# Kernel tuning notes

Measured on AMD Instinct MI355X. Metric: run time of the kernel, lower is better.

Reference implementation:

```python
import jax, jax.numpy as jnp
import numpy as np

WSIZE = 8
HEADS = 6
CYC_SHIFT = True


def _relative_index(w):
    # same math as SelfAttention._getRelativeIndex
    coords = np.stack(np.meshgrid(np.arange(w), np.arange(w), indexing='ij'))
    coords = coords.reshape(2, -1)                      # [2, w*w]
    rel = coords[:, :, None] - coords[:, None, :]       # [2, N, N]
    rel = rel.copy()
    rel[0] += w - 1
    rel[0] *= 2 * w - 1
    rel[1] += w - 1
    return (rel[0] + rel[1]).reshape(-1)                # [N*N]


def _shift_mask(H, W, w):
    # same math as CycShftWndwPartition._mask
    part = np.zeros((H, W), dtype=np.float32)
    slices = [slice(0, -w), slice(-w, -w // 2), slice(-w // 2, None)]
    idx = 0
    for hs in slices:
        for ws_ in slices:
            part[hs, ws_] = idx
            idx += 1
    part = part.reshape(H // w, w, W // w, w).transpose(0, 2, 1, 3).reshape(-1, w * w)
    diff = part[:, None, :] - part[:, :, None]          # [nW, N, N]
    return np.where(diff != 0, -100.0, 0.0).astype(np.float32)


def setup_inputs() -> dict:
    key = jax.random.key(0)
    k0, k1, k2, k3, k4 = jax.random.split(key, 5)
    B, H, W, C = 4, 384, 384, 60
    return {
        'cvrt_img': jax.random.normal(k0, (B, H, W, C), dtype=jnp.float32),
        'qkv_w': jax.random.normal(k1, (C, 3 * C), dtype=jnp.float32) * 0.05,
        'bias_matrix': jax.random.normal(k2, ((2 * WSIZE - 1) ** 2, HEADS), dtype=jnp.float32) * 0.02,
        'proj_w': jax.random.normal(k3, (C, C), dtype=jnp.float32) * 0.05,
        'proj_b': jax.random.normal(k4, (C,), dtype=jnp.float32) * 0.02,
    }


def reference(cvrt_img, qkv_w, bias_matrix, proj_w, proj_b):
    B, H, W, C = cvrt_img.shape
    w = WSIZE
    N = w * w
    d = C // HEADS
    nWh, nWw = H // w, W // w
    WNum = nWh * nWw

    # cyclic shift + window partition
    if CYC_SHIFT:
        x = jnp.roll(cvrt_img, shift=(-(w // 2), -(w // 2)), axis=(1, 2))
        mask = jnp.asarray(_shift_mask(H, W, w))        # [WNum, N, N]
    else:
        x = cvrt_img
        mask = jnp.zeros((WNum, N, N), dtype=cvrt_img.dtype)
    windows = x.reshape(B, nWh, w, nWw, w, C).transpose(0, 1, 3, 2, 4, 5)
    windows = windows.reshape(B * WNum, N, C)

    # windowed multi-head self-attention
    qkv = (windows @ qkv_w).reshape(B * WNum, N, 3, HEADS, d)
    qkv = qkv.transpose(2, 0, 3, 1, 4)                  # [3, Bw, H, N, d]
    q, k, v = qkv[0], qkv[1], qkv[2]
    attn = jnp.einsum('bhnd,bhmd->bhnm', q, k) / (d ** 0.5)

    rel_idx = jnp.asarray(_relative_index(w))
    bias = bias_matrix[rel_idx].reshape(N, N, HEADS).transpose(2, 0, 1)  # [H, N, N]
    attn = attn + bias[None]

    attn = attn.reshape(B, WNum, HEADS, N, N) + mask[None, :, None]
    attn = jax.nn.softmax(attn.reshape(B * WNum, HEADS, N, N), axis=-1)

    out = jnp.einsum('bhnm,bhmd->bhnd', attn, v)        # [Bw, H, N, d]
    out = out.transpose(0, 2, 1, 3).reshape(B * WNum, N, C)
    new_windows = out @ proj_w + proj_b

    # un-partition + reverse cyclic shift
    y = new_windows.reshape(B, nWh, nWw, w, w, C).transpose(0, 1, 3, 2, 4, 5)
    y = y.reshape(B, H, W, C)
    if CYC_SHIFT:
        y = jnp.roll(y, shift=(w // 2, w // 2), axis=(1, 2))
    return y
```

## Files before the change

kernel.cpp:

```cpp
#include <hip/hip_runtime.h>
#include <hip/hip_bf16.h>

#define IMG    384
#define CDIM   60
#define NWIN   48
#define WNUM   (NWIN * NWIN)

typedef short  bf16x8 __attribute__((ext_vector_type(8)));
typedef float  f32x4  __attribute__((ext_vector_type(4)));
union Frag { int4 i4; bf16x8 b8; };

#define MFMA(a, b, c) __builtin_amdgcn_mfma_f32_16x16x32_bf16((a), (b), (c), 0, 0, 0)

#define WS_QKVF  0
#define WS_VF    24576
#define WS_PROJF 36864
#define WS_BIASF 45056

#define SCALE_L2E (0.31622776601683794f * 1.4426950408889634f)
#define MASK_L2E  144.26950408889634f
#define LOG2E     1.4426950408889634f

__device__ __forceinline__ unsigned short f2bf(float f) {
    unsigned int u = __float_as_uint(f);
    unsigned int r = u + 0x7fffu + ((u >> 16) & 1u);
    return (unsigned short)(r >> 16);
}
__device__ __forceinline__ unsigned int pk2bf(float a, float b) {
    union { __hip_bfloat162 h; unsigned int u; } c;
    c.h = __float22bfloat162_rn(float2{a, b});
    return c.u;
}
__device__ __forceinline__ int regionOf(int x) {
    return (x < IMG - 8) ? 0 : ((x < IMG - 4) ? 1 : 2);
}
__device__ __forceinline__ int swz(int row, int byteoff) {
    return (row * 128 + byteoff) ^ ((row & 7) << 4);
}
__device__ __forceinline__ int4 qk_frag(const unsigned short* buf, int tok, int h, int g) {
    if (g == 0) return *(const int4*)((const char*)buf + swz(tok, h * 16));
    if (g == 1) {
        int v = *(const int*)((const char*)buf + swz(tok, 96 + h * 4));
        return int4{v, 0, 0, 0};
    }
    return int4{0, 0, 0, 0};
}

__global__ void swin_prep(const float* __restrict__ qw,
                          const float* __restrict__ pw,
                          const float* __restrict__ bias,
                          unsigned char* __restrict__ ws)
{
    int t = blockIdx.x * 256 + threadIdx.x;
    if (t < 1536) {
        int lane = t & 63, f = t >> 6;
        int mt = f >> 1, ks = f & 1;
        int h = mt >> 1, type = mt & 1;
        int d = lane & 15, g8 = lane >> 4;
        unsigned short v8[8];
        #pragma unroll
        for (int jj = 0; jj < 8; ++jj) {
            int c = ks * 32 + g8 * 8 + jj;
            v8[jj] = f2bf((d < 10 && c < 60) ? qw[c * 180 + type * 60 + h * 10 + d] : 0.f);
        }
        int4 p;
        p.x = v8[0] | (v8[1] << 16);  p.y = v8[2] | (v8[3] << 16);
        p.z = v8[4] | (v8[5] << 16);  p.w = v8[6] | (v8[7] << 16);
        *(int4*)(ws + WS_QKVF + t * 16) = p;
    } else if (t < 2304) {
        int t2 = t - 1536;
        int lane = t2 & 63, f = t2 >> 6;
        int h = f >> 1, ks = f & 1;
        int d = lane & 15, g8 = lane >> 4;
        unsigned short v8[8];
        #pragma unroll
        for (int jj = 0; jj < 8; ++jj) {
            int c = ks * 32 + g8 * 8 + jj;
            v8[jj] = f2bf((d < 10 && c < 60) ? qw[c * 180 + 120 + h * 10 + d] : 0.f);
        }
        int4 p;
        p.x = v8[0] | (v8[1] << 16);  p.y = v8[2] | (v8[3] << 16);
        p.z = v8[4] | (v8[5] << 16);  p.w = v8[6] | (v8[7] << 16);
        *(int4*)(ws + WS_VF + t2 * 16) = p;
    } else if (t < 2816) {
        int t2 = t - 2304;
        int lane = t2 & 63, fq = t2 >> 6;
        int m = fq >> 1, ks = fq & 1;
        int c = m * 16 + (lane & 15);
        int g8 = lane >> 4;
        unsigned short v8[8];
        #pragma unroll
        for (int jj = 0; jj < 8; ++jj) {
            int cc = ks * 32 + g8 * 8 + jj;
            v8[jj] = f2bf((c < 60 && cc < 60) ? pw[cc * 60 + c] : 0.f);
        }
        int4 p;
        p.x = v8[0] | (v8[1] << 16);  p.y = v8[2] | (v8[3] << 16);
        p.z = v8[4] | (v8[5] << 16);  p.w = v8[6] | (v8[7] << 16);
        *(int4*)(ws + WS_PROJF + t2 * 16) = p;
    } else if (t < 2816 + 24576) {
        int idx = t - 2816;
        int h = idx >> 12, r = idx & 4095;
        int i = r >> 6, j = r & 63;
        int yi = i >> 3, xi = i & 7, yj = j >> 3, xj = j & 7;
        int ridx = (yi - yj + 7) * 15 + (xi - xj + 7);
        ((float*)(ws + WS_BIASF))[h * 4096 + i * 64 + j] = bias[ridx * 6 + h] * LOG2E;
    }
}

__global__ __launch_bounds__(256, 4)
void swin_mfma(const float* __restrict__ img,
               const float* __restrict__ pbias,
               const unsigned char* __restrict__ ws,
               float* __restrict__ out)
{
    __shared__ __align__(16) unsigned short uni [64 * 64];
    __shared__ __align__(16) unsigned short qall[64 * 64];
    __shared__ __align__(16) unsigned short kall[64 * 64];
    __shared__ __align__(16) unsigned short vall[61 * 64];
    __shared__ __align__(16) unsigned short osb [64 * 64];

    const int tid  = threadIdx.x;
    const int lane = tid & 63;
    const int wid  = __builtin_amdgcn_readfirstlane(tid >> 6);
    const int l15  = lane & 15;
    const int g    = lane >> 4;
    const int dl   = (32 + l15) << 2;

    const int bid = blockIdx.x;
    const int b   = bid / WNUM;
    const int wi  = bid - b * WNUM;
    const int wh  = wi / NWIN;
    const int ww  = wi - wh * NWIN;
    const bool boundary = (wh == NWIN - 1) || (ww == NWIN - 1);

    {
        int tok = lane;
        int yi = tok >> 3, xi = tok & 7;
        int sh = wh * 8 + yi + 4; if (sh >= IMG) sh -= IMG;
        int sw = ww * 8 + xi + 4; if (sw >= IMG) sw -= IMG;
        const float* src = img + ((size_t)(b * IMG + sh) * IMG + sw) * CDIM;
        #pragma unroll
        for (int it = 0; it < 4; ++it) {
            int cg = wid + it * 4;
            if (cg < 15) {
                float4 v = *(const float4*)(src + cg * 4);
                *(int2*)((char*)uni + swz(tok, cg * 8)) =
                    make_int2(pk2bf(v.x, v.y), pk2bf(v.z, v.w));
            } else {
                *(int2*)((char*)uni + swz(tok, 120)) = make_int2(0, 0);
            }
        }
    }
    if (tid < 128) {
        int row = tid >> 1, half = tid & 1;
        *(unsigned int*)((char*)osb + swz(row, 120 + half * 4)) = 0u;
    }
    if (tid < 32) {
        *(unsigned int*)((char*)vall + swz(60, tid * 4)) = 0x3F803F80u;
    }
    __syncthreads();

    {
        Frag xb[4][2];
        #pragma unroll
        for (int n = 0; n < 4; ++n)
            #pragma unroll
            for (int ks = 0; ks < 2; ++ks)
                xb[n][ks].i4 = *(const int4*)((const char*)uni + swz(n * 16 + l15, ks * 64 + g * 16));

        const int4* wsq = (const int4*)(ws + WS_QKVF);
        #pragma unroll
        for (int kk = 0; kk < 3; ++kk) {
            int mt = wid + kk * 4;
            int h = mt >> 1, type = mt & 1;
            Frag a0, a1;
            a0.i4 = wsq[(mt * 2 + 0) * 64 + lane];
            a1.i4 = wsq[(mt * 2 + 1) * 64 + lane];
            unsigned short* dst = type ? kall : qall;
            #pragma unroll
            for (int n = 0; n < 4; ++n) {
                f32x4 acc = {0.f, 0.f, 0.f, 0.f};
                acc = MFMA(a0.b8, xb[n][0].b8, acc);
                acc = MFMA(a1.b8, xb[n][1].b8, acc);
                int tok = n * 16 + l15;
                unsigned pk01 = pk2bf(acc[0], acc[1]);
                unsigned pk23 = pk2bf(acc[2], acc[3]);
                if (g < 2)
                    *(int2*)((char*)dst + swz(tok, h * 16 + g * 8)) = make_int2(pk01, pk23);
                else if (g == 2)
                    *(unsigned*)((char*)dst + swz(tok, 96 + h * 4)) = pk01;
            }
        }
        const int4* wsv = (const int4*)(ws + WS_VF);
        int nv = (wid < 2) ? 2 : 1;
        #pragma unroll 1
        for (int kk = 0; kk < nv; ++kk) {
            int hv = wid + kk * 4;
            Frag b0, b1;
            b0.i4 = wsv[(hv * 2 + 0) * 64 + lane];
            b1.i4 = wsv[(hv * 2 + 1) * 64 + lane];
            #pragma unroll
            for (int n = 0; n < 4; ++n) {
                f32x4 acc = {0.f, 0.f, 0.f, 0.f};
                acc = MFMA(xb[n][0].b8, b0.b8, acc);
                acc = MFMA(xb[n][1].b8, b1.b8, acc);
                if (l15 < 10) {
                    *(int2*)((char*)vall + swz(hv * 10 + l15, n * 32 + g * 8)) =
                        make_int2(pk2bf(acc[0], acc[1]), pk2bf(acc[2], acc[3]));
                }
            }
        }
    }
    __syncthreads();

    const int prow = wid * 16 + l15;
    const float* biasf = (const float*)(ws + WS_BIASF);

    int h  = wid + (wid >> 1);
    int m0 = (wid & 1) * 2;
    int mc = 4 - (wid & 1) * 2;
    #pragma unroll 1
    for (int grp = 0; grp < 2; ++grp) {
        Frag kb[4];
        #pragma unroll
        for (int n = 0; n < 4; ++n)
            kb[n].i4 = qk_frag(kall, n * 16 + l15, h, g);
        int vrow = (l15 < 10) ? h * 10 + l15 : 60;
        Frag va[2];
        #pragma unroll
        for (int ks = 0; ks < 2; ++ks)
            va[ks].i4 = *(const int4*)((const char*)vall + swz(vrow, ks * 64 + g * 16));

        #pragma unroll 1
        for (int m = m0; m < m0 + mc; ++m) {
            int i_tok = m * 16 + l15;
            Frag qa;
            qa.i4 = qk_frag(qall, i_tok, h, g);

            f32x4 sacc[4];
            #pragma unroll
            for (int n = 0; n < 4; ++n) {
                f32x4 zz = {0.f, 0.f, 0.f, 0.f};
                sacc[n] = MFMA(kb[n].b8, qa.b8, zz);
            }
            const float* bp = biasf + ((h << 6) + i_tok) * 64;
            float p[4][4];
            #pragma unroll
            for (int n = 0; n < 4; ++n) {
                float4 bb = *(const float4*)(bp + n * 16 + (g << 2));
                p[n][0] = fmaf(sacc[n][0], SCALE_L2E, bb.x);
                p[n][1] = fmaf(sacc[n][1], SCALE_L2E, bb.y);
                p[n][2] = fmaf(sacc[n][2], SCALE_L2E, bb.z);
                p[n][3] = fmaf(sacc[n][3], SCALE_L2E, bb.w);
            }
            if (boundary) {
                int pi = regionOf(wh * 8 + (i_tok >> 3)) * 3 + regionOf(ww * 8 + (i_tok & 7));
                #pragma unroll
                for (int n = 0; n < 4; ++n)
                    #pragma unroll
                    for (int jj = 0; jj < 4; ++jj) {
                        int j = n * 16 + g * 4 + jj;
                        int pj = regionOf(wh * 8 + (j >> 3)) * 3 + regionOf(ww * 8 + (j & 7));
                        if (pi != pj) p[n][jj] -= MASK_L2E;
                    }
            }
            #pragma unroll
            for (int n = 0; n < 4; ++n) {
                float e0 = __builtin_exp2f(p[n][0]);
                float e1 = __builtin_exp2f(p[n][1]);
                float e2 = __builtin_exp2f(p[n][2]);
                float e3 = __builtin_exp2f(p[n][3]);
                *(int2*)((char*)uni + swz(prow, n * 32 + g * 8)) =
                    make_int2(pk2bf(e0, e1), pk2bf(e2, e3));
            }
            f32x4 pv = {0.f, 0.f, 0.f, 0.f};
            #pragma unroll
            for (int ks = 0; ks < 2; ++ks) {
                Frag pb2;
                pb2.i4 = *(const int4*)((const char*)uni + swz(prow, ks * 64 + g * 16));
                pv = MFMA(va[ks].b8, pb2.b8, pv);
            }
            float denom = __int_as_float(__builtin_amdgcn_ds_bpermute(dl, __float_as_int(pv[2])));
            float rinv  = __builtin_amdgcn_rcpf(denom);

            unsigned q01 = pk2bf(pv[0] * rinv, pv[1] * rinv);
            unsigned q23 = pk2bf(pv[2] * rinv, pv[3] * rinv);
            if (g < 2) {
                *(unsigned*)((char*)osb + swz(i_tok, h * 20 + g * 8 + 0)) = q01;
                *(unsigned*)((char*)osb + swz(i_tok, h * 20 + g * 8 + 4)) = q23;
            } else if (g == 2) {
                *(unsigned*)((char*)osb + swz(i_tok, h * 20 + 16)) = q01;
            }
        }
        h += 1; m0 = 0; mc = 6 - mc;
    }
    __syncthreads();

    {
        const int4* wsp = (const int4*)(ws + WS_PROJF);
        Frag a0, a1;
        a0.i4 = wsp[(wid * 2 + 0) * 64 + lane];
        a1.i4 = wsp[(wid * 2 + 1) * 64 + lane];
        int c0 = wid * 16 + g * 4;
        float4 pbv = (c0 < 60) ? *(const float4*)&pbias[c0] : float4{0.f, 0.f, 0.f, 0.f};
        #pragma unroll
        for (int n = 0; n < 4; ++n) {
            Frag b0, b1;
            b0.i4 = *(const int4*)((const char*)osb + swz(n * 16 + l15, g * 16));
            b1.i4 = *(const int4*)((const char*)osb + swz(n * 16 + l15, 64 + g * 16));
            f32x4 acc = {0.f, 0.f, 0.f, 0.f};
            acc = MFMA(a0.b8, b0.b8, acc);
            acc = MFMA(a1.b8, b1.b8, acc);
            if (c0 < 60) {
                int tok = n * 16 + l15;
                int yi = tok >> 3, xi = tok & 7;
                int sh = wh * 8 + yi + 4; if (sh >= IMG) sh -= IMG;
                int sw = ww * 8 + xi + 4; if (sw >= IMG) sw -= IMG;
                float4 o = {acc[0] + pbv.x, acc[1] + pbv.y, acc[2] + pbv.z, acc[3] + pbv.w};
                *(float4*)&out[((b * IMG + sh) * IMG + sw) * CDIM + c0] = o;
            }
        }
    }
}

extern "C" void kernel_launch(void* const* d_in, const int* in_sizes, int n_in,
                              void* d_out, int out_size, void* d_ws, size_t ws_size,
                              hipStream_t stream) {
    const float* img  = (const float*)d_in[0];
    const float* qw   = (const float*)d_in[1];
    const float* bias = (const float*)d_in[2];
    const float* pw   = (const float*)d_in[3];
    const float* pb   = (const float*)d_in[4];
    float* out = (float*)d_out;

    swin_prep<<<107, 256, 0, stream>>>(qw, pw, bias, (unsigned char*)d_ws);
    swin_mfma<<<4 * WNUM, 256, 0, stream>>>(img, pb,
                                            (const unsigned char*)d_ws, out);
}
```

Measured before the change: 180.7 us.

## Use six waves per window block, one attention head per wave

Raises the block from 4 to 6 wavefronts so each wave owns exactly one head through the QKV projection and the attention stage, which removes the uneven head-group loops. Q and K fragments are loaded branch-free through a shared zero buffer, and all 16 score MFMAs are issued up front. The probability slab now uses half-width staging with two PV MFMAs per row tile. The projection work is split into 12 jobs across the 6 waves. The change aims to balance work and raise occupancy, but costs more registers (sacc[4][4]) and leaves uneven projection jobs.

```diff
diff --git a/kernel.cpp b/kernel.cpp
--- a/kernel.cpp
+++ b/kernel.cpp
@@ -36,14 +36,6 @@
 }
 __device__ __forceinline__ int swz(int row, int byteoff) {
     return (row * 128 + byteoff) ^ ((row & 7) << 4);
-}
-__device__ __forceinline__ int4 qk_frag(const unsigned short* buf, int tok, int h, int g) {
-    if (g == 0) return *(const int4*)((const char*)buf + swz(tok, h * 16));
-    if (g == 1) {
-        int v = *(const int*)((const char*)buf + swz(tok, 96 + h * 4));
-        return int4{v, 0, 0, 0};
-    }
-    return int4{0, 0, 0, 0};
 }
 
 __global__ void swin_prep(const float* __restrict__ qw,
@@ -108,7 +100,7 @@
     }
 }
 
-__global__ __launch_bounds__(256, 4)
+__global__ __launch_bounds__(384, 6)
 void swin_mfma(const float* __restrict__ img,
                const float* __restrict__ pbias,
                const unsigned char* __restrict__ ws,
@@ -119,6 +111,7 @@
     __shared__ __align__(16) unsigned short kall[64 * 64];
     __shared__ __align__(16) unsigned short vall[61 * 64];
     __shared__ __align__(16) unsigned short osb [64 * 64];
+    __shared__ __align__(16) int zfrag[4];
 
     const int tid  = threadIdx.x;
     const int lane = tid & 63;
@@ -141,13 +134,13 @@
         int sw = ww * 8 + xi + 4; if (sw >= IMG) sw -= IMG;
         const float* src = img + ((size_t)(b * IMG + sh) * IMG + sw) * CDIM;
         #pragma unroll
-        for (int it = 0; it < 4; ++it) {
-            int cg = wid + it * 4;
+        for (int it = 0; it < 3; ++it) {
+            int cg = wid + it * 6;
             if (cg < 15) {
                 float4 v = *(const float4*)(src + cg * 4);
                 *(int2*)((char*)uni + swz(tok, cg * 8)) =
                     make_int2(pk2bf(v.x, v.y), pk2bf(v.z, v.w));
-            } else {
+            } else if (cg == 15) {
                 *(int2*)((char*)uni + swz(tok, 120)) = make_int2(0, 0);
             }
         }
@@ -159,6 +152,7 @@
     if (tid < 32) {
         *(unsigned int*)((char*)vall + swz(60, tid * 4)) = 0x3F803F80u;
     }
+    if (tid < 4) zfrag[tid] = 0;
     __syncthreads();
 
     {
@@ -171,9 +165,8 @@
 
         const int4* wsq = (const int4*)(ws + WS_QKVF);
         #pragma unroll
-        for (int kk = 0; kk < 3; ++kk) {
-            int mt = wid + kk * 4;
-            int h = mt >> 1, type = mt & 1;
+        for (int type = 0; type < 2; ++type) {
+            int mt = wid * 2 + type;
             Frag a0, a1;
             a0.i4 = wsq[(mt * 2 + 0) * 64 + lane];
             a1.i4 = wsq[(mt * 2 + 1) * 64 + lane];
@@ -187,72 +180,82 @@
                 unsigned pk01 = pk2bf(acc[0], acc[1]);
                 unsigned pk23 = pk2bf(acc[2], acc[3]);
                 if (g < 2)
-                    *(int2*)((char*)dst + swz(tok, h * 16 + g * 8)) = make_int2(pk01, pk23);
+                    *(int2*)((char*)dst + swz(tok, wid * 16 + g * 8)) = make_int2(pk01, pk23);
                 else if (g == 2)
-                    *(unsigned*)((char*)dst + swz(tok, 96 + h * 4)) = pk01;
+                    *(unsigned*)((char*)dst + swz(tok, 96 + wid * 4)) = pk01;
             }
         }
         const int4* wsv = (const int4*)(ws + WS_VF);
-        int nv = (wid < 2) ? 2 : 1;
-        #pragma unroll 1
-        for (int kk = 0; kk < nv; ++kk) {
-            int hv = wid + kk * 4;
-            Frag b0, b1;
-            b0.i4 = wsv[(hv * 2 + 0) * 64 + lane];
-            b1.i4 = wsv[(hv * 2 + 1) * 64 + lane];
-            #pragma unroll
-            for (int n = 0; n < 4; ++n) {
-                f32x4 acc = {0.f, 0.f, 0.f, 0.f};
-                acc = MFMA(xb[n][0].b8, b0.b8, acc);
-                acc = MFMA(xb[n][1].b8, b1.b8, acc);
-                if (l15 < 10) {
-                    *(int2*)((char*)vall + swz(hv * 10 + l15, n * 32 + g * 8)) =
-                        make_int2(pk2bf(acc[0], acc[1]), pk2bf(acc[2], acc[3]));
-                }
+        Frag b0, b1;
+        b0.i4 = wsv[(wid * 2 + 0) * 64 + lane];
+        b1.i4 = wsv[(wid * 2 + 1) * 64 + lane];
+        #pragma unroll
+        for (int n = 0; n < 4; ++n) {
+            f32x4 acc = {0.f, 0.f, 0.f, 0.f};
+            acc = MFMA(xb[n][0].b8, b0.b8, acc);
+            acc = MFMA(xb[n][1].b8, b1.b8, acc);
+            if (l15 < 10) {
+                *(int2*)((char*)vall + swz(wid * 10 + l15, n * 32 + g * 8)) =
+                    make_int2(pk2bf(acc[0], acc[1]), pk2bf(acc[2], acc[3]));
             }
         }
     }
     __syncthreads();
 
-    const int prow = wid * 16 + l15;
-    const float* biasf = (const float*)(ws + WS_BIASF);
-
-    int h  = wid + (wid >> 1);
-    int m0 = (wid & 1) * 2;
-    int mc = 4 - (wid & 1) * 2;
-    #pragma unroll 1
-    for (int grp = 0; grp < 2; ++grp) {
-        Frag kb[4];
-        #pragma unroll
-        for (int n = 0; n < 4; ++n)
-            kb[n].i4 = qk_frag(kall, n * 16 + l15, h, g);
+    {
+        const int h = wid;
+        const float* biasf = (const float*)(ws + WS_BIASF);
+        const int qb128 = swz(l15, h * 16);
+        const int qb32  = swz(l15, 96 + h * 4);
+        const bool isg0 = (g == 0), isg1 = (g == 1);
+
+        Frag kb[4], qa[4], va[2];
+        #pragma unroll
+        for (int n = 0; n < 4; ++n) {
+            const char* p128 = isg0 ? ((const char*)kall + qb128 + n * 2048) : (const char*)zfrag;
+            const char* p32  = isg1 ? ((const char*)kall + qb32  + n * 2048) : (const char*)zfrag;
+            int4 r = *(const int4*)p128;
+            r.x |= *(const int*)p32;
+            kb[n].i4 = r;
+        }
+        #pragma unroll
+        for (int m = 0; m < 4; ++m) {
+            const char* p128 = isg0 ? ((const char*)qall + qb128 + m * 2048) : (const char*)zfrag;
+            const char* p32  = isg1 ? ((const char*)qall + qb32  + m * 2048) : (const char*)zfrag;
+            int4 r = *(const int4*)p128;
+            r.x |= *(const int*)p32;
+            qa[m].i4 = r;
+        }
         int vrow = (l15 < 10) ? h * 10 + l15 : 60;
-        Frag va[2];
         #pragma unroll
         for (int ks = 0; ks < 2; ++ks)
             va[ks].i4 = *(const int4*)((const char*)vall + swz(vrow, ks * 64 + g * 16));
 
-        #pragma unroll 1
-        for (int m = m0; m < m0 + mc; ++m) {
-            int i_tok = m * 16 + l15;
-            Frag qa;
-            qa.i4 = qk_frag(qall, i_tok, h, g);
-
-            f32x4 sacc[4];
+        f32x4 sacc[4][4];
+        #pragma unroll
+        for (int m = 0; m < 4; ++m)
             #pragma unroll
             for (int n = 0; n < 4; ++n) {
                 f32x4 zz = {0.f, 0.f, 0.f, 0.f};
-                sacc[n] = MFMA(kb[n].b8, qa.b8, zz);
-            }
+                sacc[m][n] = MFMA(kb[n].b8, qa[m].b8, zz);
+            }
+
+        const int halfb = (wid >> 2) * 64;
+        const int prow  = (wid & 3) * 16 + l15;
+        char* slab = (char*)uni;
+
+        #pragma unroll
+        for (int m = 0; m < 4; ++m) {
+            int i_tok = m * 16 + l15;
             const float* bp = biasf + ((h << 6) + i_tok) * 64;
             float p[4][4];
             #pragma unroll
             for (int n = 0; n < 4; ++n) {
                 float4 bb = *(const float4*)(bp + n * 16 + (g << 2));
-                p[n][0] = fmaf(sacc[n][0], SCALE_L2E, bb.x);
-                p[n][1] = fmaf(sacc[n][1], SCALE_L2E, bb.y);
-                p[n][2] = fmaf(sacc[n][2], SCALE_L2E, bb.z);
-                p[n][3] = fmaf(sacc[n][3], SCALE_L2E, bb.w);
+                p[n][0] = fmaf(sacc[m][n][0], SCALE_L2E, bb.x);
+                p[n][1] = fmaf(sacc[m][n][1], SCALE_L2E, bb.y);
+                p[n][2] = fmaf(sacc[m][n][2], SCALE_L2E, bb.z);
+                p[n][3] = fmaf(sacc[m][n][3], SCALE_L2E, bb.w);
             }
             if (boundary) {
                 int pi = regionOf(wh * 8 + (i_tok >> 3)) * 3 + regionOf(ww * 8 + (i_tok & 7));
@@ -265,21 +268,30 @@
                         if (pi != pj) p[n][jj] -= MASK_L2E;
                     }
             }
+            unsigned w0[4], w1[4];
             #pragma unroll
             for (int n = 0; n < 4; ++n) {
                 float e0 = __builtin_exp2f(p[n][0]);
                 float e1 = __builtin_exp2f(p[n][1]);
                 float e2 = __builtin_exp2f(p[n][2]);
                 float e3 = __builtin_exp2f(p[n][3]);
-                *(int2*)((char*)uni + swz(prow, n * 32 + g * 8)) =
-                    make_int2(pk2bf(e0, e1), pk2bf(e2, e3));
+                w0[n] = pk2bf(e0, e1);
+                w1[n] = pk2bf(e2, e3);
             }
             f32x4 pv = {0.f, 0.f, 0.f, 0.f};
-            #pragma unroll
-            for (int ks = 0; ks < 2; ++ks) {
-                Frag pb2;
-                pb2.i4 = *(const int4*)((const char*)uni + swz(prow, ks * 64 + g * 16));
-                pv = MFMA(va[ks].b8, pb2.b8, pv);
+            *(int2*)(slab + swz(prow, halfb + 0 * 32 + g * 8)) = make_int2(w0[0], w1[0]);
+            *(int2*)(slab + swz(prow, halfb + 1 * 32 + g * 8)) = make_int2(w0[1], w1[1]);
+            {
+                Frag pf;
+                pf.i4 = *(const int4*)(slab + swz(prow, halfb + g * 16));
+                pv = MFMA(va[0].b8, pf.b8, pv);
+            }
+            *(int2*)(slab + swz(prow, halfb + 0 * 32 + g * 8)) = make_int2(w0[2], w1[2]);
+            *(int2*)(slab + swz(prow, halfb + 1 * 32 + g * 8)) = make_int2(w0[3], w1[3]);
+            {
+                Frag pf;
+                pf.i4 = *(const int4*)(slab + swz(prow, halfb + g * 16));
+                pv = MFMA(va[1].b8, pf.b8, pv);
             }
             float denom = __int_as_float(__builtin_amdgcn_ds_bpermute(dl, __float_as_int(pv[2])));
             float rinv  = __builtin_amdgcn_rcpf(denom);
@@ -293,32 +305,38 @@
                 *(unsigned*)((char*)osb + swz(i_tok, h * 20 + 16)) = q01;
             }
         }
-        h += 1; m0 = 0; mc = 6 - mc;
     }
     __syncthreads();
 
     {
         const int4* wsp = (const int4*)(ws + WS_PROJF);
-        Frag a0, a1;
-        a0.i4 = wsp[(wid * 2 + 0) * 64 + lane];
-        a1.i4 = wsp[(wid * 2 + 1) * 64 + lane];
-        int c0 = wid * 16 + g * 4;
-        float4 pbv = (c0 < 60) ? *(const float4*)&pbias[c0] : float4{0.f, 0.f, 0.f, 0.f};
-        #pragma unroll
-        for (int n = 0; n < 4; ++n) {
-            Frag b0, b1;
-            b0.i4 = *(const int4*)((const char*)osb + swz(n * 16 + l15, g * 16));
-            b1.i4 = *(const int4*)((const char*)osb + swz(n * 16 + l15, 64 + g * 16));
-            f32x4 acc = {0.f, 0.f, 0.f, 0.f};
-            acc = MFMA(a0.b8, b0.b8, acc);
-            acc = MFMA(a1.b8, b1.b8, acc);
-            if (c0 < 60) {
-                int tok = n * 16 + l15;
-                int yi = tok >> 3, xi = tok & 7;
-                int sh = wh * 8 + yi + 4; if (sh >= IMG) sh -= IMG;
-                int sw = ww * 8 + xi + 4; if (sw >= IMG) sw -= IMG;
-                float4 o = {acc[0] + pbv.x, acc[1] + pbv.y, acc[2] + pbv.z, acc[3] + pbv.w};
-                *(float4*)&out[((b * IMG + sh) * IMG + sw) * CDIM + c0] = o;
+        int njobs = (wid < 2) ? 2 : 1;
+        #pragma unroll 1
+        for (int j2 = 0; j2 < njobs; ++j2) {
+            int job = (j2 == 0) ? wid : 6 + wid;
+            int mt = job >> 1, nh = job & 1;
+            Frag a0, a1;
+            a0.i4 = wsp[(mt * 2 + 0) * 64 + lane];
+            a1.i4 = wsp[(mt * 2 + 1) * 64 + lane];
+            int c0 = mt * 16 + g * 4;
+            float4 pbv = (c0 < 60) ? *(const float4*)&pbias[c0] : float4{0.f, 0.f, 0.f, 0.f};
+            #pragma unroll
+            for (int nn = 0; nn < 2; ++nn) {
+                int n = nh * 2 + nn;
+                Frag b0, b1;
+                b0.i4 = *(const int4*)((const char*)osb + swz(n * 16 + l15, g * 16));
+                b1.i4 = *(const int4*)((const char*)osb + swz(n * 16 + l15, 64 + g * 16));
+                f32x4 acc = {0.f, 0.f, 0.f, 0.f};
+                acc = MFMA(a0.b8, b0.b8, acc);
+                acc = MFMA(a1.b8, b1.b8, acc);
+                if (c0 < 60) {
+                    int tok = n * 16 + l15;
+                    int yi = tok >> 3, xi = tok & 7;
+                    int sh = wh * 8 + yi + 4; if (sh >= IMG) sh -= IMG;
+                    int sw = ww * 8 + xi + 4; if (sw >= IMG) sw -= IMG;
+                    float4 o = {acc[0] + pbv.x, acc[1] + pbv.y, acc[2] + pbv.z, acc[3] + pbv.w};
+                    *(float4*)&out[((b * IMG + sh) * IMG + sw) * CDIM + c0] = o;
+                }
             }
         }
     }
@@ -335,6 +353,6 @@
     float* out = (float*)d_out;
 
     swin_prep<<<107, 256, 0, stream>>>(qw, pw, bias, (unsigned char*)d_ws);
-    swin_mfma<<<4 * WNUM, 256, 0, stream>>>(img, pb,
+    swin_mfma<<<4 * WNUM, 384, 0, stream>>>(img, pb,
                                             (const unsigned char*)d_ws, out);
 }
```

Result: slower. 325.0 us (+79.8%).

## Software-pipeline QK MFMAs across query tiles with templated fully unrolled groups

Applied to the files above, without the earlier changes.

The per-warp attention loop moves into a templated helper with a compile-time tile count, so the loop is fully unrolled and all Q fragments are preloaded. The QK^T MFMAs for the next query tile are issued before the softmax of the current tile, overlapping matrix work with exp and bias math. The P staging in LDS is halved to a 64-byte slab that is reused for the two PV k-steps. This raises register pressure (double score accumulators, preloaded Q), which may cut occupancy.

```diff
diff --git a/kernel.cpp b/kernel.cpp
--- a/kernel.cpp
+++ b/kernel.cpp
@@ -44,6 +44,109 @@
         return int4{v, 0, 0, 0};
     }
     return int4{0, 0, 0, 0};
+}
+
+template<int MC>
+__device__ __forceinline__ void attn_group(
+    int h, int m0, int l15, int g, int dl, bool boundary, int wh, int ww,
+    const unsigned short* qall, const unsigned short* kall,
+    const unsigned short* vall, unsigned short* osb,
+    char* slab, int prow, const float* biasf)
+{
+    Frag kb[4], va[2], qa[MC];
+    #pragma unroll
+    for (int n = 0; n < 4; ++n)
+        kb[n].i4 = qk_frag(kall, n * 16 + l15, h, g);
+    int vrow = (l15 < 10) ? h * 10 + l15 : 60;
+    #pragma unroll
+    for (int ks = 0; ks < 2; ++ks)
+        va[ks].i4 = *(const int4*)((const char*)vall + swz(vrow, ks * 64 + g * 16));
+    #pragma unroll
+    for (int mm = 0; mm < MC; ++mm)
+        qa[mm].i4 = qk_frag(qall, (m0 + mm) * 16 + l15, h, g);
+
+    f32x4 scur[4], snxt[4];
+    #pragma unroll
+    for (int n = 0; n < 4; ++n) {
+        f32x4 zz = {0.f, 0.f, 0.f, 0.f};
+        scur[n] = MFMA(kb[n].b8, qa[0].b8, zz);
+    }
+
+    #pragma unroll
+    for (int mm = 0; mm < MC; ++mm) {
+        int i_tok = (m0 + mm) * 16 + l15;
+
+        if (mm + 1 < MC) {
+            #pragma unroll
+            for (int n = 0; n < 4; ++n) {
+                f32x4 zz = {0.f, 0.f, 0.f, 0.f};
+                snxt[n] = MFMA(kb[n].b8, qa[mm + 1].b8, zz);
+            }
+        }
+
+        const float* bp = biasf + ((h << 6) + i_tok) * 64;
+        float p[4][4];
+        #pragma unroll
+        for (int n = 0; n < 4; ++n) {
+            float4 bb = *(const float4*)(bp + n * 16 + (g << 2));
+            p[n][0] = fmaf(scur[n][0], SCALE_L2E, bb.x);
+            p[n][1] = fmaf(scur[n][1], SCALE_L2E, bb.y);
+            p[n][2] = fmaf(scur[n][2], SCALE_L2E, bb.z);
+            p[n][3] = fmaf(scur[n][3], SCALE_L2E, bb.w);
+        }
+        if (boundary) {
+            int pi = regionOf(wh * 8 + (i_tok >> 3)) * 3 + regionOf(ww * 8 + (i_tok & 7));
+            #pragma unroll
+            for (int n = 0; n < 4; ++n)
+                #pragma unroll
+                for (int jj = 0; jj < 4; ++jj) {
+                    int j = n * 16 + g * 4 + jj;
+                    int pj = regionOf(wh * 8 + (j >> 3)) * 3 + regionOf(ww * 8 + (j & 7));
+                    if (pi != pj) p[n][jj] -= MASK_L2E;
+                }
+        }
+        unsigned w0[4], w1[4];
+        #pragma unroll
+        for (int n = 0; n < 4; ++n) {
+            float e0 = __builtin_exp2f(p[n][0]);
+            float e1 = __builtin_exp2f(p[n][1]);
+            float e2 = __builtin_exp2f(p[n][2]);
+            float e3 = __builtin_exp2f(p[n][3]);
+            w0[n] = pk2bf(e0, e1);
+            w1[n] = pk2bf(e2, e3);
+        }
+        f32x4 pv = {0.f, 0.f, 0.f, 0.f};
+        *(int2*)(slab + swz(prow, 0 * 32 + g * 8)) = make_int2(w0[0], w1[0]);
+        *(int2*)(slab + swz(prow, 1 * 32 + g * 8)) = make_int2(w0[1], w1[1]);
+        {
+            Frag pf;
+            pf.i4 = *(const int4*)(slab + swz(prow, g * 16));
+            pv = MFMA(va[0].b8, pf.b8, pv);
+        }
+        *(int2*)(slab + swz(prow, 0 * 32 + g * 8)) = make_int2(w0[2], w1[2]);
+        *(int2*)(slab + swz(prow, 1 * 32 + g * 8)) = make_int2(w0[3], w1[3]);
+        {
+            Frag pf;
+            pf.i4 = *(const int4*)(slab + swz(prow, g * 16));
+            pv = MFMA(va[1].b8, pf.b8, pv);
+        }
+        float denom = __int_as_float(__builtin_amdgcn_ds_bpermute(dl, __float_as_int(pv[2])));
+        float rinv  = __builtin_amdgcn_rcpf(denom);
+
+        unsigned q01 = pk2bf(pv[0] * rinv, pv[1] * rinv);
+        unsigned q23 = pk2bf(pv[2] * rinv, pv[3] * rinv);
+        if (g < 2) {
+            *(unsigned*)((char*)osb + swz(i_tok, h * 20 + g * 8 + 0)) = q01;
+            *(unsigned*)((char*)osb + swz(i_tok, h * 20 + g * 8 + 4)) = q23;
+        } else if (g == 2) {
+            *(unsigned*)((char*)osb + swz(i_tok, h * 20 + 16)) = q01;
+        }
+
+        if (mm + 1 < MC) {
+            #pragma unroll
+            for (int n = 0; n < 4; ++n) scur[n] = snxt[n];
+        }
+    }
 }
 
 __global__ void swin_prep(const float* __restrict__ qw,
@@ -214,86 +317,19 @@
     }
     __syncthreads();
 
-    const int prow = wid * 16 + l15;
-    const float* biasf = (const float*)(ws + WS_BIASF);
-
-    int h  = wid + (wid >> 1);
-    int m0 = (wid & 1) * 2;
-    int mc = 4 - (wid & 1) * 2;
-    #pragma unroll 1
-    for (int grp = 0; grp < 2; ++grp) {
-        Frag kb[4];
-        #pragma unroll
-        for (int n = 0; n < 4; ++n)
-            kb[n].i4 = qk_frag(kall, n * 16 + l15, h, g);
-        int vrow = (l15 < 10) ? h * 10 + l15 : 60;
-        Frag va[2];
-        #pragma unroll
-        for (int ks = 0; ks < 2; ++ks)
-            va[ks].i4 = *(const int4*)((const char*)vall + swz(vrow, ks * 64 + g * 16));
-
-        #pragma unroll 1
-        for (int m = m0; m < m0 + mc; ++m) {
-            int i_tok = m * 16 + l15;
-            Frag qa;
-            qa.i4 = qk_frag(qall, i_tok, h, g);
-
-            f32x4 sacc[4];
-            #pragma unroll
-            for (int n = 0; n < 4; ++n) {
-                f32x4 zz = {0.f, 0.f, 0.f, 0.f};
-                sacc[n] = MFMA(kb[n].b8, qa.b8, zz);
-            }
-            const float* bp = biasf + ((h << 6) + i_tok) * 64;
-            float p[4][4];
-            #pragma unroll
-            for (int n = 0; n < 4; ++n) {
-                float4 bb = *(const float4*)(bp + n * 16 + (g << 2));
-                p[n][0] = fmaf(sacc[n][0], SCALE_L2E, bb.x);
-                p[n][1] = fmaf(sacc[n][1], SCALE_L2E, bb.y);
-                p[n][2] = fmaf(sacc[n][2], SCALE_L2E, bb.z);
-                p[n][3] = fmaf(sacc[n][3], SCALE_L2E, bb.w);
-            }
-            if (boundary) {
-                int pi = regionOf(wh * 8 + (i_tok >> 3)) * 3 + regionOf(ww * 8 + (i_tok & 7));
-                #pragma unroll
-                for (int n = 0; n < 4; ++n)
-                    #pragma unroll
-                    for (int jj = 0; jj < 4; ++jj) {
-                        int j = n * 16 + g * 4 + jj;
-                        int pj = regionOf(wh * 8 + (j >> 3)) * 3 + regionOf(ww * 8 + (j & 7));
-                        if (pi != pj) p[n][jj] -= MASK_L2E;
-                    }
-            }
-            #pragma unroll
-            for (int n = 0; n < 4; ++n) {
-                float e0 = __builtin_exp2f(p[n][0]);
-                float e1 = __builtin_exp2f(p[n][1]);
-                float e2 = __builtin_exp2f(p[n][2]);
-                float e3 = __builtin_exp2f(p[n][3]);
-                *(int2*)((char*)uni + swz(prow, n * 32 + g * 8)) =
-                    make_int2(pk2bf(e0, e1), pk2bf(e2, e3));
-            }
-            f32x4 pv = {0.f, 0.f, 0.f, 0.f};
-            #pragma unroll
-            for (int ks = 0; ks < 2; ++ks) {
-                Frag pb2;
-                pb2.i4 = *(const int4*)((const char*)uni + swz(prow, ks * 64 + g * 16));
-                pv = MFMA(va[ks].b8, pb2.b8, pv);
-            }
-            float denom = __int_as_float(__builtin_amdgcn_ds_bpermute(dl, __float_as_int(pv[2])));
-            float rinv  = __builtin_amdgcn_rcpf(denom);
-
-            unsigned q01 = pk2bf(pv[0] * rinv, pv[1] * rinv);
-            unsigned q23 = pk2bf(pv[2] * rinv, pv[3] * rinv);
-            if (g < 2) {
-                *(unsigned*)((char*)osb + swz(i_tok, h * 20 + g * 8 + 0)) = q01;
-                *(unsigned*)((char*)osb + swz(i_tok, h * 20 + g * 8 + 4)) = q23;
-            } else if (g == 2) {
-                *(unsigned*)((char*)osb + swz(i_tok, h * 20 + 16)) = q01;
-            }
-        }
-        h += 1; m0 = 0; mc = 6 - mc;
+    {
+        char* slab = (char*)uni;
+        const int prow = wid * 16 + l15;
+        const float* biasf = (const float*)(ws + WS_BIASF);
+        const int h0 = wid + (wid >> 1);
+
+        if ((wid & 1) == 0) {
+            attn_group<4>(h0,     0, l15, g, dl, boundary, wh, ww, qall, kall, vall, osb, slab, prow, biasf);
+            attn_group<2>(h0 + 1, 0, l15, g, dl, boundary, wh, ww, qall, kall, vall, osb, slab, prow, biasf);
+        } else {
+            attn_group<2>(h0,     2, l15, g, dl, boundary, wh, ww, qall, kall, vall, osb, slab, prow, biasf);
+            attn_group<4>(h0 + 1, 0, l15, g, dl, boundary, wh, ww, qall, kall, vall, osb, slab, prow, biasf);
+        }
     }
     __syncthreads();
 
```

After: 180.0 us. Within noise of the previous version (-0.4%).
